# Optimization experiments

Measured on AMD Instinct MI355X. Metric: run time of the kernel, lower is better.

The kernel has to match this reference:

```python
import jax, jax.numpy as jnp
import numpy as np

N_WAY = 5
K_SHOT = 5
TEMPERATURE = 1.0
NEG = -1e9  # emulates 'column does not exist' for pad columns beyond umask_length
EPS = 1e-12  # matches torch F.normalize eps


def _l2n(x, axis):
    n = jnp.sqrt(jnp.sum(x * x, axis=axis, keepdims=True))
    return x / jnp.maximum(n, EPS)


def setup_inputs() -> dict:
    key = jax.random.key(0)
    k1, k2, k3, k4, k5 = jax.random.split(key, 5)
    b, c, h, w = 4, 64, 5, 5
    q, u = 75, 100
    support_xf = jax.random.normal(k1, (b, N_WAY * K_SHOT, c, h, w), jnp.float32)
    query_xf = jax.random.normal(k2, (b, q, c, h, w), jnp.float32)
    unlabeled_xf = jax.random.normal(k3, (b, u, c, h, w), jnp.float32)
    support_y = jax.random.randint(k4, (b, N_WAY * K_SHOT), 0, N_WAY)
    query_y = jax.random.randint(k5, (b, q), 0, N_WAY)
    return {"support_xf": support_xf, "support_y": support_y, "query_xf": query_xf,
            "query_y": query_y, "unlabeled_xf": unlabeled_xf}


def _forward(support_xf, query_xf, unlabeled_xf, query_y):
    b, q, c, h, w = query_xf.shape
    M_s = K_SHOT * h * w
    unl = unlabeled_xf.reshape(b, -1, c, h, w)
    u = unl.shape[1]
    M_u = u * h * w
    # pooled unlabeled local descriptors, flattened in (u, h, w) order -> [b, c, M_u]
    unl_feat = unl.transpose(0, 2, 1, 3, 4).reshape(b, c, M_u)
    # support -> [b, n_way, c, k_shot*h*w]
    sup = support_xf.reshape(b, N_WAY, K_SHOT, c, h, w).transpose(0, 1, 3, 2, 4, 5).reshape(b, N_WAY, c, M_s)
    # cosine similarity unlabeled -> support: [b, n_way, M_u, M_s]
    u2s = jnp.einsum('bwcn,bcm->bwmn', _l2n(sup, 2), _l2n(unl_feat, 1))
    pool = u2s.transpose(0, 2, 1, 3).reshape(b, M_u, N_WAY * M_s)
    s_nearest = jnp.argmax(pool, axis=1)          # per support loc: nearest unlabeled loc
    u_nearest = jnp.argmax(pool, axis=2)          # per unlabeled loc: nearest support loc
    mutual = jnp.take_along_axis(s_nearest, u_nearest, axis=1) == jnp.arange(M_u)[None, :]  # [b, M_u]
    # class with max similarity per unlabeled location
    cls = jnp.argmax(jnp.max(u2s, axis=-1), axis=1)  # [b, M_u]
    umask = jax.nn.one_hot(cls, N_WAY, dtype=jnp.float32).transpose(0, 2, 1) \
            * mutual[:, None, :].astype(jnp.float32)  # [b, n_way, M_u]
    counts = umask.sum(-1)                          # [b, n_way]
    L = counts.max()                                # umask_length (traced)
    # stream compaction via stable argsort of the 0/1 mask (preserves original order)
    order = jnp.argsort(-umask, axis=-1)            # jnp.argsort is stable
    pts = unl_feat.transpose(0, 2, 1)               # [b, M_u, c]
    gath = jnp.take_along_axis(pts[:, None, :, :], order[..., None], axis=2)  # [b, n_way, M_u, c]
    valid = (jnp.arange(M_u)[None, None, :] < counts[:, :, None]).astype(jnp.float32)
    comp = gath * valid[..., None]                  # rows beyond count are zeros (as in torch)
    s_cat = jnp.concatenate([sup, comp.transpose(0, 1, 3, 2)], axis=-1)  # [b, n_way, c, M_s+M_u]
    M_tot = M_s + M_u
    qn = _l2n(query_xf.reshape(b, q, c, h * w), 2)
    scn = _l2n(s_cat, 2)
    sim = jnp.einsum('bqcm,bwcn->bqwmn', qn, scn)   # [b, q, n_way, M_q, M_tot]
    sim = (sim + 1.0) * 0.5                          # FourLayer_64F branch
    # columns beyond umask_length don't exist in the torch dense tensor -> exclude from maxes
    pad = jnp.arange(M_tot)[None, None, None, None, :] >= (M_s + L)
    sim = jnp.where(pad, NEG, sim)
    M_q = h * w
    qm = sim.transpose(0, 1, 3, 2, 4).reshape(b, q, M_q, N_WAY * M_tot)
    support_nearest = jnp.argmax(qm, axis=2)        # [b, q, n_way*M_tot]
    query_nearest = jnp.argmax(qm, axis=3)          # [b, q, M_q]
    g = jnp.take_along_axis(support_nearest, query_nearest, axis=2)
    q_mask = (g == jnp.arange(M_q)[None, None, :]).astype(sim.dtype)  # mutual NN mask
    query_value = (jnp.max(sim, axis=-1) * q_mask[:, :, None, :]).sum(-1)  # [b, q, n_way]
    logits = query_value.reshape(b * q, N_WAY) / TEMPERATURE
    y = query_y.reshape(b * q)
    logp = jax.nn.log_softmax(logits, axis=-1)
    loss = -jnp.take_along_axis(logp, y[:, None], axis=1).mean()
    return loss


def reference(support_xf, support_y, query_xf, query_y, unlabeled_xf):
    return _forward(support_xf, query_xf, unlabeled_xf, query_y)
```

## Files before the change

kernel.cpp:

```cpp
#include <hip/hip_runtime.h>

#define NEGINF (-1e30f)

constexpr size_t OF_UNL  = 0;
constexpr size_t OF_SUP  = OF_UNL  + (size_t)4*2500*64;
constexpr size_t OF_SUPT = OF_SUP  + (size_t)4*5*125*64;
constexpr size_t OF_QT   = OF_SUPT + (size_t)4*5*64*128;
constexpr size_t OF_ROWV = OF_QT   + (size_t)300*28*64;
constexpr size_t OF_UKEY = OF_ROWV;
constexpr size_t OF_SKEY = OF_ROWV + 20000;
constexpr size_t OF_CBQ  = OF_ROWV + 25000;
constexpr size_t OF_CVI  = OF_ROWV + (size_t)2*4*5*8*2500;
constexpr size_t OF_CMP  = OF_CVI  + (size_t)4*5*125*20*2;
constexpr size_t OF_CNT  = OF_CMP  + (size_t)4*5*2500;
constexpr size_t OF_UNEAR= OF_CNT  + 20;
constexpr size_t OF_SNEAR= OF_UNEAR+ 10000;
constexpr size_t OF_BV   = OF_SNEAR+ 2500;
constexpr size_t OF_BP   = OF_BV   + 37500;
constexpr size_t OF_AMX  = OF_BP   + 37500;

typedef __attribute__((ext_vector_type(4)))  float f4s;
typedef __attribute__((ext_vector_type(16))) float f16s;

__device__ __forceinline__ unsigned long long pack_key(float v, int idx) {
    unsigned int e = __float_as_uint(v);
    e ^= (e >> 31) ? 0xFFFFFFFFu : 0x80000000u;
    return ((unsigned long long)e << 32) | (unsigned int)~idx;
}

__global__ __launch_bounds__(256) void knorm(
    const float* __restrict__ sup, const float* __restrict__ qry,
    const float* __restrict__ unl, float* __restrict__ ws,
    float* __restrict__ out)
{
    float* unl_n = ws + OF_UNL;
    float* sup_n = ws + OF_SUP;
    float* supT  = ws + OF_SUPT;
    float* qt    = ws + OF_QT;

    int tid = threadIdx.x;
    int lane = tid & 63, wv = tid >> 6;
    int gid = blockIdx.x * 256 + tid;

    if (gid == 0) *out = 0.f;
    if (gid < 25300) ((unsigned int*)(ws + OF_UKEY))[gid] = 0u;

    int unit = blockIdx.x * 4 + wv;

    __shared__ float ls[4][1600];
    __shared__ float scl[4][32];

    const float* src;
    float* dstT; float* dst2 = nullptr; int dst2_shot = 0; bool isq = false;

    if (unit < 400) {
        int b = unit / 100, u = unit % 100;
        src  = unl + (size_t)unit * 1600;
        dstT = unl_n + ((size_t)(b * 2500 + u * 25)) * 64;
    } else if (unit < 500) {
        int idx2 = unit - 400;
        int b = idx2 / 25, r = idx2 % 25;
        int w = r / 5, shot = r % 5;
        src  = sup + (size_t)(b * 25 + r) * 1600;
        dstT = sup_n + ((size_t)(b * 625 + w * 125 + shot * 25)) * 64;
        dst2 = supT + ((size_t)(b * 5 + w) * 64) * 128;
        dst2_shot = shot * 25;
    } else {
        int bq = unit - 500;
        src  = qry + (size_t)bq * 1600;
        dstT = qt + (size_t)bq * 1792;
        isq = true;
    }

    const float4* s4 = (const float4*)src;
#pragma unroll
    for (int k = 0; k < 7; ++k) {
        int idx = k * 64 + lane;
        if (idx < 400) *(float4*)&ls[wv][idx * 4] = s4[idx];
    }
    __syncthreads();

    if (lane < 25) {
        int hw = lane;
        float p[16];
#pragma unroll
        for (int sub = 0; sub < 16; ++sub) {
            float s = 0.f;
#pragma unroll
            for (int j = 0; j < 4; ++j) {
                float v = ls[wv][(sub * 4 + j) * 25 + hw];
                s += v * v;
            }
            p[sub] = s;
        }
#pragma unroll
        for (int st = 1; st < 16; st <<= 1)
#pragma unroll
            for (int i = 0; i < 16; i += 2 * st)
                p[i] = p[i] + p[i + st];
        scl[wv][hw] = 1.f / fmaxf(sqrtf(p[0]), 1e-12f);
    }
    __syncthreads();

    float4* d4 = (float4*)dstT;
#pragma unroll
    for (int k = 0; k < 7; ++k) {
        int idx = k * 64 + lane;
        if (idx < 400) {
            int f = idx * 4;
            int r_ = f >> 6;
            int c0 = f & 63;
            float m = scl[wv][r_];
            float4 o;
            o.x = ls[wv][ c0      * 25 + r_] * m;
            o.y = ls[wv][(c0 + 1) * 25 + r_] * m;
            o.z = ls[wv][(c0 + 2) * 25 + r_] * m;
            o.w = ls[wv][(c0 + 3) * 25 + r_] * m;
            d4[idx] = o;
        }
    }
    if (isq && lane < 48) d4[400 + lane] = make_float4(0.f, 0.f, 0.f, 0.f);
    if (dst2) {
#pragma unroll
        for (int k = 0; k < 25; ++k) {
            int idx = k * 64 + lane;
            int c = idx / 25, hw2 = idx % 25;
            dst2[(size_t)c * 128 + dst2_shot + hw2] = ls[wv][idx] * scl[wv][hw2];
        }
    }
}

#define KB2(C) { \
    f16s s0, s1; \
    asm volatile("s_load_dwordx16 %0, %[b], %c[o0]\n\t" \
                 "s_load_dwordx16 %1, %[b], %c[o1]\n\t" \
                 "s_waitcnt lgkmcnt(0)" \
                 : "=s"(s0), "=s"(s1) \
                 : [b]"s"(sbp), [o0]"i"((C)*512), [o1]"i"((C)*512+512)); \
    float2 uv = *(const float2*)&uls[ml * 66 + (C)]; \
    acc[0]  = fmaf(uv.x, s0[0],  fmaf(uv.y, s1[0],  acc[0])); \
    acc[1]  = fmaf(uv.x, s0[1],  fmaf(uv.y, s1[1],  acc[1])); \
    acc[2]  = fmaf(uv.x, s0[2],  fmaf(uv.y, s1[2],  acc[2])); \
    acc[3]  = fmaf(uv.x, s0[3],  fmaf(uv.y, s1[3],  acc[3])); \
    acc[4]  = fmaf(uv.x, s0[4],  fmaf(uv.y, s1[4],  acc[4])); \
    acc[5]  = fmaf(uv.x, s0[5],  fmaf(uv.y, s1[5],  acc[5])); \
    acc[6]  = fmaf(uv.x, s0[6],  fmaf(uv.y, s1[6],  acc[6])); \
    acc[7]  = fmaf(uv.x, s0[7],  fmaf(uv.y, s1[7],  acc[7])); \
    acc[8]  = fmaf(uv.x, s0[8],  fmaf(uv.y, s1[8],  acc[8])); \
    acc[9]  = fmaf(uv.x, s0[9],  fmaf(uv.y, s1[9],  acc[9])); \
    acc[10] = fmaf(uv.x, s0[10], fmaf(uv.y, s1[10], acc[10])); \
    acc[11] = fmaf(uv.x, s0[11], fmaf(uv.y, s1[11], acc[11])); \
    acc[12] = fmaf(uv.x, s0[12], fmaf(uv.y, s1[12], acc[12])); \
    acc[13] = fmaf(uv.x, s0[13], fmaf(uv.y, s1[13], acc[13])); \
    acc[14] = fmaf(uv.x, s0[14], fmaf(uv.y, s1[14], acc[14])); \
    acc[15] = fmaf(uv.x, s0[15], fmaf(uv.y, s1[15], acc[15])); }
#define KB8(C) KB2(C) KB2((C)+2) KB2((C)+4) KB2((C)+6)

__global__ __launch_bounds__(256) void kb(
    const float* __restrict__ unl_n, const float* __restrict__ supT,
    unsigned long long* __restrict__ ukey, unsigned long long* __restrict__ skey)
{
    int bid = blockIdx.x;
    int nc = bid & 3;
    int mb = (bid >> 2) % 20;
    int bw = bid / 80;
    int b  = bw / 5;
    int w  = bw % 5;
    int tid = threadIdx.x;
    int lane = tid & 63, wv = tid >> 6;

    __shared__ float uls[128 * 66];
    __shared__ float sv_[4][32];
    __shared__ int   si_[4][32];

    int m0 = mb * 128;
    int n0 = nc * 32;

    for (int i = tid; i < 128 * 16; i += 256) {
        int row = i >> 4, c4 = (i & 15) * 4;
        int m = m0 + row;
        float4 x = make_float4(0.f, 0.f, 0.f, 0.f);
        if (m < 2500) x = *(const float4*)(unl_n + ((size_t)(b * 2500 + m)) * 64 + c4);
        *(float2*)&uls[row * 66 + c4]     = make_float2(x.x, x.y);
        *(float2*)&uls[row * 66 + c4 + 2] = make_float2(x.z, x.w);
    }
    __syncthreads();

    int ml = tid & 127;
    int m  = m0 + ml;
    int nh = tid >> 7;
    int nbase = nh * 16;
    int nbu = __builtin_amdgcn_readfirstlane(nbase);
    int nn_total = (125 - n0) < 32 ? (125 - n0) : 32;
    const float* sbp = supT + ((size_t)bw * 64) * 128 + n0 + nbu;

    float acc[16];
#pragma unroll
    for (int j = 0; j < 16; ++j) acc[j] = 0.f;

    KB8(0)  KB8(8)  KB8(16) KB8(24)
    KB8(32) KB8(40) KB8(48) KB8(56)

    int nnloc = nn_total - nbase;
    nnloc = nnloc < 0 ? 0 : (nnloc > 16 ? 16 : nnloc);
    float rbv = NEGINF; int rbi = 0;
    for (int j = 0; j < nnloc; ++j)
        if (acc[j] > rbv) { rbv = acc[j]; rbi = n0 + nbase + j; }
    if (m < 2500)
        atomicMax(ukey + (b * 2500 + m), pack_key(rbv, w * 125 + rbi));

#pragma unroll
    for (int j = 0; j < 16; ++j) {
        float v = (m < 2500 && (nbase + j) < nn_total) ? acc[j] : NEGINF;
        float vm = v;
#pragma unroll
        for (int s2 = 1; s2 < 64; s2 <<= 1) vm = fmaxf(vm, __shfl_xor(vm, s2));
        unsigned long long msk = __ballot(v == vm);
        int first = __ffsll((unsigned long long)msk) - 1;
        if (lane == 0) { sv_[wv][nbase + j] = vm; si_[wv][nbase + j] = m0 + (wv & 1) * 64 + first; }
    }
    __syncthreads();
    if (tid < nn_total) {
        int w0 = (tid < 16) ? 0 : 2;
        float v = sv_[w0][tid];     int vi = si_[w0][tid];
        float v2 = sv_[w0 + 1][tid]; int i2 = si_[w0 + 1][tid];
        if (v2 > v || (v2 == v && i2 < vi)) { v = v2; vi = i2; }
        atomicMax(skey + (bw * 125 + n0 + tid), pack_key(v, vi));
    }
}

__global__ __launch_bounds__(256) void kcmp(
    const unsigned long long* __restrict__ ukey,
    const unsigned long long* __restrict__ skey,
    int* __restrict__ cmp, int* __restrict__ cntg)
{
    int p = blockIdx.x;
    int b = p / 5, way = p % 5;
    int tid = threadIdx.x, lane = tid & 63, wv = tid >> 6;
    __shared__ unsigned long long masks[40];
    __shared__ int base[40];

    for (int ch = wv; ch < 40; ch += 4) {
        int m = ch * 64 + lane;
        bool ok = false;
        if (m < 2500) {
            int un = (int)(~(unsigned int)ukey[b * 2500 + m]);
            ok = (un / 125 == way) &&
                 ((int)(~(unsigned int)skey[b * 625 + un]) == m);
        }
        unsigned long long msk = __ballot(ok ? 1 : 0);
        if (lane == 0) masks[ch] = msk;
    }
    __syncthreads();
    if (tid == 0) {
        int s = 0;
        for (int ch = 0; ch < 40; ++ch) { base[ch] = s; s += __popcll(masks[ch]); }
        cntg[p] = s;
    }
    __syncthreads();
    for (int ch = wv; ch < 40; ch += 4) {
        unsigned long long msk = masks[ch];
        if ((msk >> lane) & 1ull) {
            int pre = __popcll(msk & ((1ull << lane) - 1ull));
            cmp[(size_t)p * 2500 + base[ch] + pre] = ch * 64 + lane;
        }
    }
}

#define QLOAD(CG, Q0,Q1,Q2,Q3,Q4,Q5,Q6) \
  asm volatile( \
    "s_load_dwordx4 %0, %[b], %c[o0]\n\t" \
    "s_load_dwordx4 %1, %[b], %c[o1]\n\t" \
    "s_load_dwordx4 %2, %[b], %c[o2]\n\t" \
    "s_load_dwordx4 %3, %[b], %c[o3]\n\t" \
    "s_load_dwordx4 %4, %[b], %c[o4]\n\t" \
    "s_load_dwordx4 %5, %[b], %c[o5]\n\t" \
    "s_load_dwordx4 %6, %[b], %c[o6]\n\t" \
    "s_waitcnt lgkmcnt(0)" \
    : "=s"(Q0), "=s"(Q1), "=s"(Q2), "=s"(Q3), "=s"(Q4), "=s"(Q5), "=s"(Q6) \
    : [b]"s"(qbp), \
      [o0]"i"((CG)*16 + 0*256), [o1]"i"((CG)*16 + 1*256), \
      [o2]"i"((CG)*16 + 2*256), [o3]"i"((CG)*16 + 3*256), \
      [o4]"i"((CG)*16 + 4*256), [o5]"i"((CG)*16 + 5*256), \
      [o6]"i"((CG)*16 + 6*256))

#define CGSTEP(CG) { \
    f4s q0,q1,q2,q3,q4,q5,q6; \
    QLOAD(CG, q0,q1,q2,q3,q4,q5,q6); \
    float4 cl = *(const float4*)&cls[lane * 68 + (CG) * 4]; \
    acc[0]=fmaf(q0.x,cl.x,fmaf(q0.y,cl.y,fmaf(q0.z,cl.z,fmaf(q0.w,cl.w,acc[0])))); \
    acc[1]=fmaf(q1.x,cl.x,fmaf(q1.y,cl.y,fmaf(q1.z,cl.z,fmaf(q1.w,cl.w,acc[1])))); \
    acc[2]=fmaf(q2.x,cl.x,fmaf(q2.y,cl.y,fmaf(q2.z,cl.z,fmaf(q2.w,cl.w,acc[2])))); \
    acc[3]=fmaf(q3.x,cl.x,fmaf(q3.y,cl.y,fmaf(q3.z,cl.z,fmaf(q3.w,cl.w,acc[3])))); \
    acc[4]=fmaf(q4.x,cl.x,fmaf(q4.y,cl.y,fmaf(q4.z,cl.z,fmaf(q4.w,cl.w,acc[4])))); \
    acc[5]=fmaf(q5.x,cl.x,fmaf(q5.y,cl.y,fmaf(q5.z,cl.z,fmaf(q5.w,cl.w,acc[5])))); \
    acc[6]=fmaf(q6.x,cl.x,fmaf(q6.y,cl.y,fmaf(q6.z,cl.z,fmaf(q6.w,cl.w,acc[6])))); }

#define ASTORE_F(P, V) __hip_atomic_store((P), (V), __ATOMIC_RELAXED, __HIP_MEMORY_SCOPE_AGENT)
#define ASTORE_I(P, V) __hip_atomic_store((P), (V), __ATOMIC_RELAXED, __HIP_MEMORY_SCOPE_AGENT)
#define ALOAD(P)       __hip_atomic_load((P), __ATOMIC_RELAXED, __HIP_MEMORY_SCOPE_AGENT)

__global__ __launch_bounds__(256) void kc1(
    const float* __restrict__ qt, const float* __restrict__ sup_n,
    const float* __restrict__ unl_n, const int* __restrict__ cmp,
    const int* __restrict__ cntg,
    float* __restrict__ bvg, int* __restrict__ bpg,
    unsigned char* __restrict__ amaxg, int* __restrict__ cntbq,
    const int* __restrict__ qy, float* __restrict__ out)
{
    int bid = blockIdx.x;
    int w = bid % 5, bq = bid / 5;
    int b = bq / 75;
    int tid = threadIdx.x;
    int lane = tid & 63;
    int wvu = __builtin_amdgcn_readfirstlane(tid >> 6);
    int pbw = b * 5 + w;

    int L = 0;
#pragma unroll
    for (int i = 0; i < 20; ++i) { int v = cntg[i]; L = L > v ? L : v; }
    int cntw = 0, wb = 0;
#pragma unroll
    for (int w2 = 0; w2 < 5; ++w2) {
        int c2 = cntg[b * 5 + w2];
        if (w2 < w) wb += 125 + c2;
        if (w2 == w) cntw = c2;
    }
    int cw = 125 + cntw;

    __shared__ float cls[64 * 68];
    __shared__ float amxv[4][64];
    __shared__ int   amxg_[4][64];
    __shared__ float redv[25];
    __shared__ int   redn[25];
    __shared__ int   lastf;
    __shared__ float qmask[25];
    __shared__ float lg[5];

    const float* qbp = qt + ((size_t)bq * 28 + wvu * 7) * 64;

    float rv[7]; int rn[7];
#pragma unroll
    for (int j = 0; j < 7; ++j) { rv[j] = NEGINF; rn[j] = 0x7fffffff; }

    int nb = (cw + 63) >> 6;

    for (int b4 = 0; b4 < nb; ++b4) {
        if (b4 > 0 && tid < 64) {
            int n = (b4 - 1) * 64 + tid;
            if (n < cw) {
                float v = amxv[0][tid]; int g = amxg_[0][tid];
#pragma unroll
                for (int g2 = 1; g2 < 4; ++g2)
                    if (amxv[g2][tid] > v) { v = amxv[g2][tid]; g = amxg_[g2][tid]; }
                ASTORE_I(&amaxg[(size_t)bq * 3200 + (wb + n)], (unsigned char)g);
            }
        }
#pragma unroll
        for (int k = 0; k < 4; ++k) {
            int i = tid + k * 256;
            int row = i >> 4, ch = i & 15;
            int n = b4 * 64 + row;
            float4 x = make_float4(0.f, 0.f, 0.f, 0.f);
            if (n < cw) {
                const float* cp;
                if (n < 125) cp = sup_n + (((size_t)pbw) * 125 + n) * 64;
                else { int m = cmp[((size_t)pbw) * 2500 + (n - 125)];
                       cp = unl_n + ((size_t)(b * 2500 + m)) * 64; }
                x = *(const float4*)(cp + ch * 4);
            }
            *(float4*)&cls[row * 68 + ch * 4] = x;
        }
        __syncthreads();

        float acc[7];
#pragma unroll
        for (int j = 0; j < 7; ++j) acc[j] = 0.f;

        CGSTEP(0);  CGSTEP(1);  CGSTEP(2);  CGSTEP(3);
        CGSTEP(4);  CGSTEP(5);  CGSTEP(6);  CGSTEP(7);
        CGSTEP(8);  CGSTEP(9);  CGSTEP(10); CGSTEP(11);
        CGSTEP(12); CGSTEP(13); CGSTEP(14); CGSTEP(15);

        bool colvalid = (b4 * 64 + lane) < cw;
        float cmax = NEGINF; int cam = 0;
#pragma unroll
        for (int j = 0; j < 7; ++j) {
            int mq = wvu * 7 + j;
            float s = (acc[j] + 1.0f) * 0.5f;
            float sm = (colvalid && mq < 25) ? s : NEGINF;
            if (sm > cmax) { cmax = sm; cam = mq; }
            float vm = sm;
#pragma unroll
            for (int t = 1; t < 64; t <<= 1) vm = fmaxf(vm, __shfl_xor(vm, t));
            unsigned long long msk = __ballot(sm == vm);
            int first = __ffsll(msk) - 1;
            if (vm > rv[j]) { rv[j] = vm; rn[j] = b4 * 64 + first; }
        }
        amxv[wvu][lane] = cmax; amxg_[wvu][lane] = cam;
        __syncthreads();
    }

    if (tid < 64) {
        int n = (nb - 1) * 64 + tid;
        if (n < cw) {
            float v = amxv[0][tid]; int g = amxg_[0][tid];
#pragma unroll
            for (int g2 = 1; g2 < 4; ++g2)
                if (amxv[g2][tid] > v) { v = amxv[g2][tid]; g = amxg_[g2][tid]; }
            ASTORE_I(&amaxg[(size_t)bq * 3200 + (wb + n)], (unsigned char)g);
        }
    }
    if (lane == 0) {
#pragma unroll
        for (int j = 0; j < 7; ++j) {
            int mq = wvu * 7 + j;
            if (mq < 25) { redv[mq] = rv[j]; redn[mq] = rn[j]; }
        }
    }
    __syncthreads();

    if (tid < 25) {
        float v = redv[tid]; int nn = redn[tid];
        int p = ((w * 2625 + nn) << 12) | (wb + nn);
        if (L > cntw) {
            int pp = ((w * 2625 + 125 + cntw) << 12) | 0xFFF;
            if (0.5f > v || (0.5f == v && pp < p)) { v = 0.5f; p = pp; }
        }
        size_t o = ((size_t)bq * 5 + w) * 25 + tid;
        ASTORE_F(&bvg[o], v); ASTORE_I(&bpg[o], p);
    }

    asm volatile("s_waitcnt vmcnt(0)" ::: "memory");
    if (tid == 0)
        lastf = (__hip_atomic_fetch_add(cntbq + bq, 1, __ATOMIC_RELAXED,
                                        __HIP_MEMORY_SCOPE_AGENT) == 4) ? 1 : 0;
    __syncthreads();
    if (!lastf) return;

    if (tid < 25) {
        float v = NEGINF; int p = 0x7fffffff;
#pragma unroll
        for (int w2 = 0; w2 < 5; ++w2) {
            size_t o = ((size_t)bq * 5 + w2) * 25 + tid;
            float v2 = ALOAD(&bvg[o]);
            int   p2 = ALOAD(&bpg[o]);
            if (v2 > v || (v2 == v && p2 < p)) { v = v2; p = p2; }
        }
        int pos = p & 0xFFF;
        int g = 0;
        if (pos != 0xFFF)
            g = (int)ALOAD(&amaxg[(size_t)bq * 3200 + pos]);
        qmask[tid] = (g == tid) ? 1.0f : 0.0f;
    }
    __syncthreads();
    if (tid < 5) {
        float s = 0.f;
#pragma unroll
        for (int mq = 0; mq < 25; ++mq) {
            size_t o = ((size_t)bq * 5 + tid) * 25 + mq;
            s += ALOAD(&bvg[o]) * qmask[mq];
        }
        lg[tid] = s;
    }
    __syncthreads();
    if (tid == 0) {
        int y = qy[bq];
        float mx = lg[0];
#pragma unroll
        for (int w2 = 1; w2 < 5; ++w2) mx = fmaxf(mx, lg[w2]);
        float se = 0.f;
#pragma unroll
        for (int w2 = 0; w2 < 5; ++w2) se += expf(lg[w2] - mx);
        float loss = -(lg[y] - mx - logf(se));
        atomicAdd(out, loss * (1.0f / 300.0f));
    }
}

extern "C" void kernel_launch(void* const* d_in, const int* in_sizes, int n_in,
                              void* d_out, int out_size, void* d_ws, size_t ws_size,
                              hipStream_t stream)
{
    const float* sup = (const float*)d_in[0];
    const float* qry = (const float*)d_in[2];
    const int*   qy  = (const int*)d_in[3];
    const float* unl = (const float*)d_in[4];

    float* ws    = (float*)d_ws;
    float* unl_n = ws + OF_UNL;
    float* sup_n = ws + OF_SUP;
    float* supT  = ws + OF_SUPT;
    float* qt    = ws + OF_QT;
    unsigned long long* ukey = (unsigned long long*)(ws + OF_UKEY);
    unsigned long long* skey = (unsigned long long*)(ws + OF_SKEY);
    int*   cntbq = (int*)(ws + OF_CBQ);
    int*   cmp   = (int*)(ws + OF_CMP);
    int*   cntg  = (int*)(ws + OF_CNT);
    float* bvg   = ws + OF_BV;
    int*   bpg   = (int*)(ws + OF_BP);
    unsigned char* amaxg = (unsigned char*)(ws + OF_AMX);

    hipLaunchKernelGGL(knorm, dim3(200), dim3(256), 0, stream,
                       sup, qry, unl, ws, (float*)d_out);
    hipLaunchKernelGGL(kb, dim3(1600), dim3(256), 0, stream,
                       unl_n, supT, ukey, skey);
    hipLaunchKernelGGL(kcmp, dim3(20), dim3(256), 0, stream,
                       ukey, skey, cmp, cntg);
    hipLaunchKernelGGL(kc1, dim3(1500), dim3(256), 0, stream,
                       qt, sup_n, unl_n, cmp, cntg, bvg, bpg, amaxg,
                       cntbq, qy, (float*)d_out);
}
```

Baseline: 154.7 us.

## Fuse mutual-NN compaction kernel into kc1 via global flag spin-wait

Removes the separate kcmp launch. The first 20 blocks of kc1 now do the mutual-nearest compaction, publish the counts, and bump a global counter that knorm zeroes. Every kc1 block then spins on that flag before reading the counts. This saves one kernel launch and its gap, but all 1500 blocks wait on the first 20, and correctness depends on those blocks being scheduled first. The compaction writes use relaxed atomics with no release or acquire fence, so visibility is not strictly guaranteed.

```diff
diff --git a/kernel.cpp b/kernel.cpp
--- a/kernel.cpp
+++ b/kernel.cpp
@@ -10,6 +10,7 @@
 constexpr size_t OF_UKEY = OF_ROWV;
 constexpr size_t OF_SKEY = OF_ROWV + 20000;
 constexpr size_t OF_CBQ  = OF_ROWV + 25000;
+constexpr size_t OF_FLAG = OF_ROWV + 25300;
 constexpr size_t OF_CVI  = OF_ROWV + (size_t)2*4*5*8*2500;
 constexpr size_t OF_CMP  = OF_CVI  + (size_t)4*5*125*20*2;
 constexpr size_t OF_CNT  = OF_CMP  + (size_t)4*5*2500;
@@ -27,6 +28,10 @@
     e ^= (e >> 31) ? 0xFFFFFFFFu : 0x80000000u;
     return ((unsigned long long)e << 32) | (unsigned int)~idx;
 }
+
+#define ASTORE_F(P, V) __hip_atomic_store((P), (V), __ATOMIC_RELAXED, __HIP_MEMORY_SCOPE_AGENT)
+#define ASTORE_I(P, V) __hip_atomic_store((P), (V), __ATOMIC_RELAXED, __HIP_MEMORY_SCOPE_AGENT)
+#define ALOAD(P)       __hip_atomic_load((P), __ATOMIC_RELAXED, __HIP_MEMORY_SCOPE_AGENT)
 
 __global__ __launch_bounds__(256) void knorm(
     const float* __restrict__ sup, const float* __restrict__ qry,
@@ -43,7 +48,7 @@
     int gid = blockIdx.x * 256 + tid;
 
     if (gid == 0) *out = 0.f;
-    if (gid < 25300) ((unsigned int*)(ws + OF_UKEY))[gid] = 0u;
+    if (gid < 25301) ((unsigned int*)(ws + OF_UKEY))[gid] = 0u;
 
     int unit = blockIdx.x * 4 + wv;
 
@@ -229,44 +234,6 @@
     }
 }
 
-__global__ __launch_bounds__(256) void kcmp(
-    const unsigned long long* __restrict__ ukey,
-    const unsigned long long* __restrict__ skey,
-    int* __restrict__ cmp, int* __restrict__ cntg)
-{
-    int p = blockIdx.x;
-    int b = p / 5, way = p % 5;
-    int tid = threadIdx.x, lane = tid & 63, wv = tid >> 6;
-    __shared__ unsigned long long masks[40];
-    __shared__ int base[40];
-
-    for (int ch = wv; ch < 40; ch += 4) {
-        int m = ch * 64 + lane;
-        bool ok = false;
-        if (m < 2500) {
-            int un = (int)(~(unsigned int)ukey[b * 2500 + m]);
-            ok = (un / 125 == way) &&
-                 ((int)(~(unsigned int)skey[b * 625 + un]) == m);
-        }
-        unsigned long long msk = __ballot(ok ? 1 : 0);
-        if (lane == 0) masks[ch] = msk;
-    }
-    __syncthreads();
-    if (tid == 0) {
-        int s = 0;
-        for (int ch = 0; ch < 40; ++ch) { base[ch] = s; s += __popcll(masks[ch]); }
-        cntg[p] = s;
-    }
-    __syncthreads();
-    for (int ch = wv; ch < 40; ch += 4) {
-        unsigned long long msk = masks[ch];
-        if ((msk >> lane) & 1ull) {
-            int pre = __popcll(msk & ((1ull << lane) - 1ull));
-            cmp[(size_t)p * 2500 + base[ch] + pre] = ch * 64 + lane;
-        }
-    }
-}
-
 #define QLOAD(CG, Q0,Q1,Q2,Q3,Q4,Q5,Q6) \
   asm volatile( \
     "s_load_dwordx4 %0, %[b], %c[o0]\n\t" \
@@ -296,14 +263,12 @@
     acc[5]=fmaf(q5.x,cl.x,fmaf(q5.y,cl.y,fmaf(q5.z,cl.z,fmaf(q5.w,cl.w,acc[5])))); \
     acc[6]=fmaf(q6.x,cl.x,fmaf(q6.y,cl.y,fmaf(q6.z,cl.z,fmaf(q6.w,cl.w,acc[6])))); }
 
-#define ASTORE_F(P, V) __hip_atomic_store((P), (V), __ATOMIC_RELAXED, __HIP_MEMORY_SCOPE_AGENT)
-#define ASTORE_I(P, V) __hip_atomic_store((P), (V), __ATOMIC_RELAXED, __HIP_MEMORY_SCOPE_AGENT)
-#define ALOAD(P)       __hip_atomic_load((P), __ATOMIC_RELAXED, __HIP_MEMORY_SCOPE_AGENT)
-
 __global__ __launch_bounds__(256) void kc1(
     const float* __restrict__ qt, const float* __restrict__ sup_n,
-    const float* __restrict__ unl_n, const int* __restrict__ cmp,
-    const int* __restrict__ cntg,
+    const float* __restrict__ unl_n,
+    const unsigned long long* __restrict__ ukey,
+    const unsigned long long* __restrict__ skey,
+    int* __restrict__ cmp, int* __restrict__ cntg, int* __restrict__ flag,
     float* __restrict__ bvg, int* __restrict__ bpg,
     unsigned char* __restrict__ amaxg, int* __restrict__ cntbq,
     const int* __restrict__ qy, float* __restrict__ out)
@@ -313,20 +278,9 @@
     int b = bq / 75;
     int tid = threadIdx.x;
     int lane = tid & 63;
+    int wvk = tid >> 6;
     int wvu = __builtin_amdgcn_readfirstlane(tid >> 6);
     int pbw = b * 5 + w;
-
-    int L = 0;
-#pragma unroll
-    for (int i = 0; i < 20; ++i) { int v = cntg[i]; L = L > v ? L : v; }
-    int cntw = 0, wb = 0;
-#pragma unroll
-    for (int w2 = 0; w2 < 5; ++w2) {
-        int c2 = cntg[b * 5 + w2];
-        if (w2 < w) wb += 125 + c2;
-        if (w2 == w) cntw = c2;
-    }
-    int cw = 125 + cntw;
 
     __shared__ float cls[64 * 68];
     __shared__ float amxv[4][64];
@@ -336,6 +290,57 @@
     __shared__ int   lastf;
     __shared__ float qmask[25];
     __shared__ float lg[5];
+
+    if (bid < 20) {
+        int pb = bid / 5, pway = bid % 5;
+        unsigned long long* masks = (unsigned long long*)cls;
+        int* basep = (int*)(cls + 80);
+
+        for (int ch = wvk; ch < 40; ch += 4) {
+            int m = ch * 64 + lane;
+            bool ok = false;
+            if (m < 2500) {
+                int un = (int)(~(unsigned int)ukey[pb * 2500 + m]);
+                ok = (un / 125 == pway) &&
+                     ((int)(~(unsigned int)skey[pb * 625 + un]) == m);
+            }
+            unsigned long long msk = __ballot(ok ? 1 : 0);
+            if (lane == 0) masks[ch] = msk;
+        }
+        __syncthreads();
+        if (tid == 0) {
+            int s = 0;
+            for (int ch = 0; ch < 40; ++ch) { basep[ch] = s; s += __popcll(masks[ch]); }
+            ASTORE_I(&cntg[bid], s);
+        }
+        __syncthreads();
+        for (int ch = wvk; ch < 40; ch += 4) {
+            unsigned long long msk = masks[ch];
+            if ((msk >> lane) & 1ull) {
+                int pre = __popcll(msk & ((1ull << lane) - 1ull));
+                ASTORE_I(&cmp[(size_t)bid * 2500 + basep[ch] + pre], ch * 64 + lane);
+            }
+        }
+        __syncthreads();
+        if (tid == 0)
+            __hip_atomic_fetch_add(flag, 1, __ATOMIC_RELAXED, __HIP_MEMORY_SCOPE_AGENT);
+    }
+    if (tid == 0) {
+        while (ALOAD(flag) != 20) __builtin_amdgcn_s_sleep(8);
+    }
+    __syncthreads();
+
+    int L = 0;
+#pragma unroll
+    for (int i = 0; i < 20; ++i) { int v = cntg[i]; L = L > v ? L : v; }
+    int cntw = 0, wb = 0;
+#pragma unroll
+    for (int w2 = 0; w2 < 5; ++w2) {
+        int c2 = cntg[b * 5 + w2];
+        if (w2 < w) wb += 125 + c2;
+        if (w2 == w) cntw = c2;
+    }
+    int cw = 125 + cntw;
 
     const float* qbp = qt + ((size_t)bq * 28 + wvu * 7) * 64;
 
@@ -494,6 +499,7 @@
     unsigned long long* ukey = (unsigned long long*)(ws + OF_UKEY);
     unsigned long long* skey = (unsigned long long*)(ws + OF_SKEY);
     int*   cntbq = (int*)(ws + OF_CBQ);
+    int*   flag  = (int*)(ws + OF_FLAG);
     int*   cmp   = (int*)(ws + OF_CMP);
     int*   cntg  = (int*)(ws + OF_CNT);
     float* bvg   = ws + OF_BV;
@@ -504,9 +510,7 @@
                        sup, qry, unl, ws, (float*)d_out);
     hipLaunchKernelGGL(kb, dim3(1600), dim3(256), 0, stream,
                        unl_n, supT, ukey, skey);
-    hipLaunchKernelGGL(kcmp, dim3(20), dim3(256), 0, stream,
-                       ukey, skey, cmp, cntg);
     hipLaunchKernelGGL(kc1, dim3(1500), dim3(256), 0, stream,
-                       qt, sup_n, unl_n, cmp, cntg, bvg, bpg, amaxg,
-                       cntbq, qy, (float*)d_out);
+                       qt, sup_n, unl_n, ukey, skey, cmp, cntg, flag,
+                       bvg, bpg, amaxg, cntbq, qy, (float*)d_out);
 }
```

New measurement: 156.4 us. No clear change (+1.1%).
